# Kernel optimization log

Hardware: AMD Instinct MI355X
Metric: run time of the kernel (lower is better)

## Reference

```python
import jax, jax.numpy as jnp
import numpy as np

INPUT_DIM = 512
HIDDEN_DIM = 256
REP_DIM = 256
SCORE_HIDDEN = 128


def setup_inputs() -> dict:
    key = jax.random.key(0)
    ks = jax.random.split(key, 12)
    def rn(k, shape, scale=None):
        s = scale if scale is not None else 1.0 / np.sqrt(shape[0])
        return jax.random.normal(k, shape, dtype=jnp.float32) * s
    return {
        "feat_x": jax.random.normal(ks[0], (512, INPUT_DIM), dtype=jnp.float32),
        "feat_pos": jax.random.normal(ks[1], (512, INPUT_DIM), dtype=jnp.float32),
        "feat_neg": jax.random.normal(ks[2], (512, INPUT_DIM), dtype=jnp.float32),
        # g: Linear(input,hidden) -> GELU -> Linear(hidden,rep); stored as x @ W
        "g_w1": rn(ks[3], (INPUT_DIM, HIDDEN_DIM)),
        "g_b1": jnp.zeros((HIDDEN_DIM,), jnp.float32),
        "g_w2": rn(ks[4], (HIDDEN_DIM, REP_DIM)),
        "g_b2": jnp.zeros((REP_DIM,), jnp.float32),
        # out_proj: Linear(rep, input, bias=False)
        "out_w": rn(ks[5], (REP_DIM, INPUT_DIM)),
        # score_net: Linear(3*rep+1, score_hidden) -> GELU -> Linear(score_hidden, 1)
        "s_w1": rn(ks[6], (3 * REP_DIM + 1, SCORE_HIDDEN)),
        "s_b1": jnp.zeros((SCORE_HIDDEN,), jnp.float32),
        "s_w2": rn(ks[7], (SCORE_HIDDEN, 1)),
        "s_b2": jnp.zeros((1,), jnp.float32),
    }


def _gelu(x):
    return jax.nn.gelu(x, approximate=False)  # torch nn.GELU default = exact erf


def _g(x, g_w1, g_b1, g_w2, g_b2):
    return _gelu(x @ g_w1 + g_b1) @ g_w2 + g_b2


def _set_operator(feat_x, feat_set, params):
    g_w1, g_b1, g_w2, g_b2, out_w, s_w1, s_b1, s_w2, s_b2 = params
    x_rep = _g(feat_x, g_w1, g_b1, g_w2, g_b2)   # (n, r)
    y_rep = _g(feat_set, g_w1, g_b1, g_w2, g_b2)  # (m, r)
    n, r = x_rep.shape
    m = y_rep.shape[0]
    x_exp = jnp.broadcast_to(x_rep[:, None, :], (n, m, r))
    y_exp = jnp.broadcast_to(y_rep[None, :, :], (n, m, r))
    delta = y_exp - x_exp                                   # (n, m, r)
    delta_norm = jnp.linalg.norm(delta, axis=-1, keepdims=True)
    score_in = jnp.concatenate([x_exp, y_exp, delta, delta_norm], axis=-1)  # (n, m, 3r+1)
    logits = (_gelu(score_in @ s_w1 + s_b1) @ s_w2 + s_b2)[..., 0]          # (n, m)
    weights = jax.nn.softmax(logits, axis=1)
    set_update_rep = jnp.einsum("nm,nmr->nr", weights, delta)
    return set_update_rep @ out_w


def reference(feat_x, feat_pos, feat_neg, g_w1, g_b1, g_w2, g_b2, out_w, s_w1, s_b1, s_w2, s_b2):
    params = (g_w1, g_b1, g_w2, g_b2, out_w, s_w1, s_b1, s_w2, s_b2)
    s_pos = _set_operator(feat_x, feat_pos, params)
    s_neg = _set_operator(feat_x, feat_neg, params)  # mask_self_neg=False
    return s_pos - s_neg
```

## Files before the change

kernel.cpp:

```cpp
#include <hip/hip_runtime.h>
#include <math.h>

#define NN 512
#define IN 512
#define HD 256
#define RD 256
#define SH 128

__device__ __forceinline__ float gelu_fast(float x){
    const float z  = x * 0.70710678118654752f;
    const float az = fabsf(z);
    const float t  = __builtin_amdgcn_rcpf(fmaf(0.3275911f, az, 1.0f));
    float p = fmaf(1.061405429f, t, -1.453152027f);
    p = fmaf(p, t, 1.421413741f);
    p = fmaf(p, t, -0.284496736f);
    p = fmaf(p, t, 0.254829592f);
    p = p * t;
    const float e = __builtin_amdgcn_exp2f(z * z * -1.4426950408889634f);
    const float E = p * e;
    const float one_plus_erf = (x >= 0.0f) ? (2.0f - E) : E;
    return 0.5f * x * one_plus_erf;
}

__device__ __forceinline__ float gelu2(float u){
    const float az = fabsf(u);
    const float tt = __builtin_amdgcn_rcpf(fmaf(0.23166045f, az, 1.0f));
    float p = fmaf(1.061405429f, tt, -1.453152027f);
    p = fmaf(p, tt, 1.421413741f);
    p = fmaf(p, tt, -0.284496736f);
    p = fmaf(p, tt, 0.254829592f);
    p = p * tt;
    const float e2 = __builtin_amdgcn_exp2f(u * u * -0.72134752044448170f);
    const float Eq = p * e2;
    const float ope = (u >= 0.0f) ? (2.0f - Eq) : Eq;
    return u * ope;
}

__global__ __launch_bounds__(512) void k_rep(
    const float* __restrict__ fx, const float* __restrict__ fp, const float* __restrict__ fn,
    const float* __restrict__ w1, const float* __restrict__ b1,
    const float* __restrict__ w2, const float* __restrict__ b2,
    const float* __restrict__ s_w1,
    float* __restrict__ r_x, float* __restrict__ r_p, float* __restrict__ r_n,
    float* __restrict__ rT_p, float* __restrict__ rT_n,
    float* __restrict__ A_x, float* __restrict__ BT_p, float* __restrict__ BT_n)
{
    __shared__ float xs[4][IN];
    __shared__ float ps[8][4][HD];
    __shared__ float hs[4][HD];
    __shared__ float rloc[4][RD];
    __shared__ float ab4[4][SH];
    const int t = threadIdx.x;
    const int mat = blockIdx.x >> 7;
    const int row0 = (blockIdx.x & 127) << 2;
    const float* src = (mat==0) ? fx : (mat==1) ? fp : fn;

    {
        const int j = t >> 7, c4 = (t & 127) << 2;
        *(float4*)&xs[j][c4] = *(const float4*)&src[(row0+j)*IN + c4];
    }
    __syncthreads();

    const int cg = t & 63, s = t >> 6;
    const int c0 = cg << 2;

    {
        float4 acc[4];
        #pragma unroll
        for (int j=0;j<4;j++) acc[j] = make_float4(0.f,0.f,0.f,0.f);
        const float* wp = w1 + (s*64)*HD + c0;
        #pragma unroll 8
        for (int ii=0; ii<64; ii++){
            float4 w = *(const float4*)wp; wp += HD;
            const int i = s*64 + ii;
            #pragma unroll
            for (int j=0;j<4;j++){
                const float xv = xs[j][i];
                acc[j].x = fmaf(xv, w.x, acc[j].x);
                acc[j].y = fmaf(xv, w.y, acc[j].y);
                acc[j].z = fmaf(xv, w.z, acc[j].z);
                acc[j].w = fmaf(xv, w.w, acc[j].w);
            }
        }
        #pragma unroll
        for (int j=0;j<4;j++) *(float4*)&ps[s][j][c0] = acc[j];
    }
    __syncthreads();

    #pragma unroll
    for (int rep=0; rep<2; rep++){
        const int idx = rep*512 + t;
        const int j = idx >> 8, c = idx & 255;
        float v = b1[c];
        #pragma unroll
        for (int ss=0; ss<8; ss++) v += ps[ss][j][c];
        hs[j][c] = gelu_fast(v);
    }
    __syncthreads();

    {
        float4 acc[4];
        #pragma unroll
        for (int j=0;j<4;j++) acc[j] = make_float4(0.f,0.f,0.f,0.f);
        const float* wp = w2 + (s*32)*RD + c0;
        #pragma unroll 8
        for (int ii=0; ii<32; ii++){
            float4 w = *(const float4*)wp; wp += RD;
            const int i = s*32 + ii;
            #pragma unroll
            for (int j=0;j<4;j++){
                const float xv = hs[j][i];
                acc[j].x = fmaf(xv, w.x, acc[j].x);
                acc[j].y = fmaf(xv, w.y, acc[j].y);
                acc[j].z = fmaf(xv, w.z, acc[j].z);
                acc[j].w = fmaf(xv, w.w, acc[j].w);
            }
        }
        #pragma unroll
        for (int j=0;j<4;j++) *(float4*)&ps[s][j][c0] = acc[j];
    }
    __syncthreads();

    float* rout = (mat==0) ? r_x : (mat==1) ? r_p : r_n;
    #pragma unroll
    for (int rep=0; rep<2; rep++){
        const int idx = rep*512 + t;
        const int j = idx >> 8, c = idx & 255;
        float v = b2[c];
        #pragma unroll
        for (int ss=0; ss<8; ss++) v += ps[ss][j][c];
        rloc[j][c] = v;
        rout[(row0+j)*RD + c] = v;
    }
    __syncthreads();

    if (mat && t < 256){
        float* rT = (mat==1) ? rT_p : rT_n;
        float4 q = make_float4(rloc[0][t], rloc[1][t], rloc[2][t], rloc[3][t]);
        *(float4*)&rT[t*NN + row0] = q;
    }

    {
        const int cg2 = t & 31, s2 = t >> 5;
        const int cc0 = cg2 << 2;
        const float sgn = (mat==0) ? -1.0f : 1.0f;
        const int base1 = (mat==0) ? 0 : 256;
        const float* p1 = s_w1 + (base1 + s2*16)*SH + cc0;
        const float* p3 = s_w1 + (512   + s2*16)*SH + cc0;
        float4 a[4];
        #pragma unroll
        for (int j=0;j<4;j++) a[j] = make_float4(0.f,0.f,0.f,0.f);
        #pragma unroll 8
        for (int ii=0; ii<16; ii++){
            float4 wa = *(const float4*)p1; p1 += SH;
            float4 wd = *(const float4*)p3; p3 += SH;
            float4 w;
            w.x = fmaf(sgn, wd.x, wa.x);
            w.y = fmaf(sgn, wd.y, wa.y);
            w.z = fmaf(sgn, wd.z, wa.z);
            w.w = fmaf(sgn, wd.w, wa.w);
            const int i = s2*16 + ii;
            #pragma unroll
            for (int j=0;j<4;j++){
                const float xv = rloc[j][i];
                a[j].x = fmaf(xv, w.x, a[j].x);
                a[j].y = fmaf(xv, w.y, a[j].y);
                a[j].z = fmaf(xv, w.z, a[j].z);
                a[j].w = fmaf(xv, w.w, a[j].w);
            }
        }
        float* psf = &ps[0][0][0];
        #pragma unroll
        for (int j=0;j<4;j++) *(float4*)&psf[(s2*4 + j)*SH + cc0] = a[j];
    }
    __syncthreads();

    {
        const float* psf = &ps[0][0][0];
        const int j = t >> 7, c = t & 127;
        float v = 0.f;
        #pragma unroll
        for (int ss=0; ss<16; ss++) v += psf[(ss*4 + j)*SH + c];
        if (mat==0) A_x[(row0+j)*SH + c] = v;
        else        ab4[j][c] = v;
    }
    __syncthreads();
    if (mat && t < 128){
        float* BT = (mat==1) ? BT_p : BT_n;
        float4 q = make_float4(ab4[0][t], ab4[1][t], ab4[2][t], ab4[3][t]);
        *(float4*)&BT[t*NN + row0] = q;
    }
}

__global__ __launch_bounds__(256) void k_sd(
    const float* __restrict__ r_x, const float* __restrict__ rT_p, const float* __restrict__ rT_n,
    const float* __restrict__ A_x, const float* __restrict__ BT_p, const float* __restrict__ BT_n,
    const float* __restrict__ r_p, const float* __restrict__ r_n,
    const float* __restrict__ s_w1, const float* __restrict__ s_b1,
    const float* __restrict__ s_w2,
    float* __restrict__ psum, float* __restrict__ Spart)
{
    __shared__ float2 xs2[RD];
    __shared__ float4 cmb[SH];
    __shared__ float pda[2][128];
    __shared__ float pdb[2][128];
    __shared__ float pdc[2][128];
    __shared__ float2 evb[128];
    __shared__ float nx[2];
    __shared__ float ssum[2][2];
    const int t = threadIdx.x;
    const int set = blockIdx.x >> 10;
    const int rem = blockIdx.x & 1023;
    const int n0 = (rem >> 2) << 1;
    const int mt = rem & 3;
    const int mbase = mt << 7;
    const int tm = t & 127, kh = t >> 7;
    const int m = mbase + tm;
    const float* yT = set ? rT_n : rT_p;
    const float* BT = set ? BT_n : BT_p;

    xs2[t] = make_float2(r_x[n0*RD + t], r_x[(n0+1)*RD + t]);
    if (t < SH){
        const float b1v = s_b1[t];
        cmb[t] = make_float4(A_x[n0*SH + t] + b1v,
                             A_x[(n0+1)*SH + t] + b1v,
                             s_w1[768*SH + t],
                             0.5f * s_w2[t]);
    }
    __syncthreads();

    if (t < 128){
        const int w = t >> 6, l = t & 63;
        float v = 0.f;
        #pragma unroll
        for (int q=0;q<4;q++){
            const float2 e = xs2[l + 64*q];
            const float ev = w ? e.y : e.x;
            v = fmaf(ev, ev, v);
        }
        #pragma unroll
        for (int off=32; off>=1; off>>=1) v += __shfl_xor(v, off);
        if (l==0) nx[w] = v;
    }

    float d0=0.f, d1=0.f, ny=0.f;
    {
        const float* yp = yT + (kh << 7)*NN + m;
        #pragma unroll 16
        for (int rr=0; rr<128; rr++){
            const float y = yp[rr*NN];
            const float2 xv = xs2[(kh << 7) + rr];
            d0 = fmaf(xv.x, y, d0);
            d1 = fmaf(xv.y, y, d1);
            ny = fmaf(y, y, ny);
        }
    }
    pda[kh][tm] = d0; pdb[kh][tm] = d1; pdc[kh][tm] = ny;
    __syncthreads();
    d0 += pda[1-kh][tm]; d1 += pdb[1-kh][tm]; ny += pdc[1-kh][tm];
    const float dn0 = sqrtf(fmaxf(fmaf(-2.f, d0, nx[0] + ny), 0.f));
    const float dn1 = sqrtf(fmaxf(fmaf(-2.f, d1, nx[1] + ny), 0.f));

    float acc0 = 0.f, acc1 = 0.f;
    {
        const float* bp = BT + (kh << 6)*NN + m;
        #pragma unroll 4
        for (int kk=0; kk<64; kk++){
            const float b = bp[kk*NN];
            const float4 c = cmb[(kh << 6) + kk];
            const float u0 = fmaf(dn0, c.z, c.x + b);
            const float u1 = fmaf(dn1, c.z, c.y + b);
            acc0 = fmaf(c.w, gelu2(u0), acc0);
            acc1 = fmaf(c.w, gelu2(u1), acc1);
        }
    }
    __syncthreads();
    pda[kh][tm] = acc0; pdb[kh][tm] = acc1;
    __syncthreads();
    if (kh == 0){
        const float ev0 = __builtin_amdgcn_exp2f((acc0 + pda[1][tm]) * 1.4426950408889634f);
        const float ev1 = __builtin_amdgcn_exp2f((acc1 + pdb[1][tm]) * 1.4426950408889634f);
        evb[tm] = make_float2(ev0, ev1);
        float v0 = ev0, v1 = ev1;
        #pragma unroll
        for (int off=32; off>=1; off>>=1){ v0 += __shfl_xor(v0, off); v1 += __shfl_xor(v1, off); }
        if ((t & 63) == 0){
            ssum[tm >> 6][0] = v0;
            ssum[tm >> 6][1] = v1;
        }
    }
    __syncthreads();
    if (t < 2)
        Spart[(set*4 + mt)*NN + n0 + t] = ssum[0][t] + ssum[1][t];

    {
        const float* ry = (set ? r_n : r_p) + mbase*RD + t;
        float a0 = 0.f, a1 = 0.f;
        #pragma unroll 8
        for (int mm=0; mm<128; mm++){
            const float rv = ry[mm*RD];
            const float2 w = evb[mm];
            a0 = fmaf(w.x, rv, a0);
            a1 = fmaf(w.y, rv, a1);
        }
        float* P = psum + ((set*4 + mt)*NN + n0)*RD;
        P[t]      = a0;
        P[RD + t] = a1;
    }
}

__global__ __launch_bounds__(512) void k_fin(
    const float* __restrict__ psum, const float* __restrict__ Spart,
    const float* __restrict__ out_w, float* __restrict__ out)
{
    __shared__ float dv[2][RD];
    const int t = threadIdx.x;
    const int np = blockIdx.x >> 1, ch = blockIdx.x & 1;
    const int n0 = np << 1;

    {
        const int j = t >> 8, c = t & 255;
        const int n = n0 + j;
        float Sp = 0.f, Sn = 0.f;
        #pragma unroll
        for (int q=0;q<4;q++){
            Sp += Spart[q*NN + n];
            Sn += Spart[(4+q)*NN + n];
        }
        float vp = 0.f, vn = 0.f;
        #pragma unroll
        for (int q=0;q<4;q++){
            vp += psum[(q*NN + n)*RD + c];
            vn += psum[((4+q)*NN + n)*RD + c];
        }
        dv[j][c] = vp * (1.0f/Sp) - vn * (1.0f/Sn);
    }
    __syncthreads();

    {
        const int j = t >> 8, col = (ch << 8) + (t & 255);
        float o = 0.f;
        const float* wo = out_w + col;
        #pragma unroll 8
        for (int r=0; r<RD; r++){ o = fmaf(dv[j][r], *wo, o); wo += IN; }
        out[(n0+j)*IN + col] = o;
    }
}

extern "C" void kernel_launch(void* const* d_in, const int* in_sizes, int n_in,
                              void* d_out, int out_size, void* d_ws, size_t ws_size,
                              hipStream_t stream)
{
    const float* fx  = (const float*)d_in[0];
    const float* fp  = (const float*)d_in[1];
    const float* fn  = (const float*)d_in[2];
    const float* gw1 = (const float*)d_in[3];
    const float* gb1 = (const float*)d_in[4];
    const float* gw2 = (const float*)d_in[5];
    const float* gb2 = (const float*)d_in[6];
    const float* ow  = (const float*)d_in[7];
    const float* sw1 = (const float*)d_in[8];
    const float* sb1 = (const float*)d_in[9];
    const float* sw2 = (const float*)d_in[10];
    float* out = (float*)d_out;

    float* ws   = (float*)d_ws;
    float* r_x  = ws;
    float* r_p  = r_x  + 131072;
    float* r_n  = r_p  + 131072;
    float* rT_p = r_n  + 131072;
    float* rT_n = rT_p + 131072;
    float* A_x  = rT_n + 131072;
    float* BT_p = A_x  + 65536;
    float* BT_n = BT_p + 65536;
    float* Spar = BT_n + 65536;
    float* psum = Spar + 4096;

    hipLaunchKernelGGL(k_rep, dim3(384), dim3(512), 0, stream,
                       fx, fp, fn, gw1, gb1, gw2, gb2, sw1,
                       r_x, r_p, r_n, rT_p, rT_n, A_x, BT_p, BT_n);
    hipLaunchKernelGGL(k_sd, dim3(2048), dim3(256), 0, stream,
                       r_x, rT_p, rT_n, A_x, BT_p, BT_n, r_p, r_n,
                       sw1, sb1, sw2, psum, Spar);
    hipLaunchKernelGGL(k_fin, dim3(512), dim3(512), 0, stream,
                       psum, Spar, ow, out);
}
```

Measured before the change: 159.3 us.

## Precompute squared norms in rep kernel, halve rows per block, cheaper GELU polynomial

```diff
diff --git a/kernel.cpp b/kernel.cpp
--- a/kernel.cpp
+++ b/kernel.cpp
@@ -24,120 +24,113 @@
 
 __device__ __forceinline__ float gelu2(float u){
     const float az = fabsf(u);
-    const float tt = __builtin_amdgcn_rcpf(fmaf(0.23166045f, az, 1.0f));
-    float p = fmaf(1.061405429f, tt, -1.453152027f);
-    p = fmaf(p, tt, 1.421413741f);
-    p = fmaf(p, tt, -0.284496736f);
-    p = fmaf(p, tt, 0.254829592f);
-    p = p * tt;
+    const float tt = __builtin_amdgcn_rcpf(fmaf(0.3326725f, az, 1.0f));
+    const float P  = fmaf(fmaf(0.7478556f, tt, -0.0958798f), tt, 0.3480242f) * tt;
     const float e2 = __builtin_amdgcn_exp2f(u * u * -0.72134752044448170f);
-    const float Eq = p * e2;
+    const float Eq = P * e2;
     const float ope = (u >= 0.0f) ? (2.0f - Eq) : Eq;
     return u * ope;
 }
 
-__global__ __launch_bounds__(512) void k_rep(
+__global__ __launch_bounds__(512, 6) void k_rep(
     const float* __restrict__ fx, const float* __restrict__ fp, const float* __restrict__ fn,
     const float* __restrict__ w1, const float* __restrict__ b1,
     const float* __restrict__ w2, const float* __restrict__ b2,
     const float* __restrict__ s_w1,
     float* __restrict__ r_x, float* __restrict__ r_p, float* __restrict__ r_n,
     float* __restrict__ rT_p, float* __restrict__ rT_n,
-    float* __restrict__ A_x, float* __restrict__ BT_p, float* __restrict__ BT_n)
+    float* __restrict__ A_x, float* __restrict__ BT_p, float* __restrict__ BT_n,
+    float* __restrict__ nx2, float* __restrict__ np2, float* __restrict__ nn2)
 {
-    __shared__ float xs[4][IN];
-    __shared__ float ps[8][4][HD];
-    __shared__ float hs[4][HD];
-    __shared__ float rloc[4][RD];
-    __shared__ float ab4[4][SH];
+    __shared__ float2 xs2[IN];
+    __shared__ float ps[8][2][HD];
+    __shared__ float2 hs2[HD];
+    __shared__ float2 rl2[RD];
+    __shared__ float ab2[2][SH];
     const int t = threadIdx.x;
-    const int mat = blockIdx.x >> 7;
-    const int row0 = (blockIdx.x & 127) << 2;
+    const int mat = blockIdx.x >> 8;
+    const int row0 = (blockIdx.x & 255) << 1;
     const float* src = (mat==0) ? fx : (mat==1) ? fp : fn;
 
-    {
-        const int j = t >> 7, c4 = (t & 127) << 2;
-        *(float4*)&xs[j][c4] = *(const float4*)&src[(row0+j)*IN + c4];
-    }
+    xs2[t] = make_float2(src[row0*IN + t], src[(row0+1)*IN + t]);
     __syncthreads();
 
     const int cg = t & 63, s = t >> 6;
     const int c0 = cg << 2;
 
     {
-        float4 acc[4];
-        #pragma unroll
-        for (int j=0;j<4;j++) acc[j] = make_float4(0.f,0.f,0.f,0.f);
+        float4 a0 = make_float4(0.f,0.f,0.f,0.f), a1 = a0;
         const float* wp = w1 + (s*64)*HD + c0;
         #pragma unroll 8
         for (int ii=0; ii<64; ii++){
-            float4 w = *(const float4*)wp; wp += HD;
-            const int i = s*64 + ii;
-            #pragma unroll
-            for (int j=0;j<4;j++){
-                const float xv = xs[j][i];
-                acc[j].x = fmaf(xv, w.x, acc[j].x);
-                acc[j].y = fmaf(xv, w.y, acc[j].y);
-                acc[j].z = fmaf(xv, w.z, acc[j].z);
-                acc[j].w = fmaf(xv, w.w, acc[j].w);
-            }
-        }
-        #pragma unroll
-        for (int j=0;j<4;j++) *(float4*)&ps[s][j][c0] = acc[j];
-    }
-    __syncthreads();
-
-    #pragma unroll
-    for (int rep=0; rep<2; rep++){
-        const int idx = rep*512 + t;
-        const int j = idx >> 8, c = idx & 255;
+            const float4 w = *(const float4*)wp; wp += HD;
+            const float2 x = xs2[s*64 + ii];
+            a0.x = fmaf(x.x, w.x, a0.x); a0.y = fmaf(x.x, w.y, a0.y);
+            a0.z = fmaf(x.x, w.z, a0.z); a0.w = fmaf(x.x, w.w, a0.w);
+            a1.x = fmaf(x.y, w.x, a1.x); a1.y = fmaf(x.y, w.y, a1.y);
+            a1.z = fmaf(x.y, w.z, a1.z); a1.w = fmaf(x.y, w.w, a1.w);
+        }
+        *(float4*)&ps[s][0][c0] = a0;
+        *(float4*)&ps[s][1][c0] = a1;
+    }
+    __syncthreads();
+
+    {
+        const int j = t >> 8, c = t & 255;
         float v = b1[c];
         #pragma unroll
         for (int ss=0; ss<8; ss++) v += ps[ss][j][c];
-        hs[j][c] = gelu_fast(v);
-    }
-    __syncthreads();
-
-    {
-        float4 acc[4];
-        #pragma unroll
-        for (int j=0;j<4;j++) acc[j] = make_float4(0.f,0.f,0.f,0.f);
+        ((float*)hs2)[c*2 + j] = gelu_fast(v);
+    }
+    __syncthreads();
+
+    {
+        float4 a0 = make_float4(0.f,0.f,0.f,0.f), a1 = a0;
         const float* wp = w2 + (s*32)*RD + c0;
         #pragma unroll 8
         for (int ii=0; ii<32; ii++){
-            float4 w = *(const float4*)wp; wp += RD;
-            const int i = s*32 + ii;
-            #pragma unroll
-            for (int j=0;j<4;j++){
-                const float xv = hs[j][i];
-                acc[j].x = fmaf(xv, w.x, acc[j].x);
-                acc[j].y = fmaf(xv, w.y, acc[j].y);
-                acc[j].z = fmaf(xv, w.z, acc[j].z);
-                acc[j].w = fmaf(xv, w.w, acc[j].w);
-            }
-        }
-        #pragma unroll
-        for (int j=0;j<4;j++) *(float4*)&ps[s][j][c0] = acc[j];
-    }
-    __syncthreads();
-
-    float* rout = (mat==0) ? r_x : (mat==1) ? r_p : r_n;
-    #pragma unroll
-    for (int rep=0; rep<2; rep++){
-        const int idx = rep*512 + t;
-        const int j = idx >> 8, c = idx & 255;
+            const float4 w = *(const float4*)wp; wp += RD;
+            const float2 x = hs2[s*32 + ii];
+            a0.x = fmaf(x.x, w.x, a0.x); a0.y = fmaf(x.x, w.y, a0.y);
+            a0.z = fmaf(x.x, w.z, a0.z); a0.w = fmaf(x.x, w.w, a0.w);
+            a1.x = fmaf(x.y, w.x, a1.x); a1.y = fmaf(x.y, w.y, a1.y);
+            a1.z = fmaf(x.y, w.z, a1.z); a1.w = fmaf(x.y, w.w, a1.w);
+        }
+        *(float4*)&ps[s][0][c0] = a0;
+        *(float4*)&ps[s][1][c0] = a1;
+    }
+    __syncthreads();
+
+    {
+        const int j = t >> 8, c = t & 255;
         float v = b2[c];
         #pragma unroll
         for (int ss=0; ss<8; ss++) v += ps[ss][j][c];
-        rloc[j][c] = v;
+        ((float*)rl2)[c*2 + j] = v;
+        float* rout = (mat==0) ? r_x : (mat==1) ? r_p : r_n;
         rout[(row0+j)*RD + c] = v;
     }
     __syncthreads();
 
+    if (t < 128){
+        const int w = t >> 6, l = t & 63;
+        float v = 0.f;
+        #pragma unroll
+        for (int q=0;q<4;q++){
+            const float2 e = rl2[l + 64*q];
+            const float ev = w ? e.y : e.x;
+            v = fmaf(ev, ev, v);
+        }
+        #pragma unroll
+        for (int off=32; off>=1; off>>=1) v += __shfl_xor(v, off);
+        if (l==0){
+            float* nrm = (mat==0) ? nx2 : (mat==1) ? np2 : nn2;
+            nrm[row0 + w] = v;
+        }
+    }
     if (mat && t < 256){
         float* rT = (mat==1) ? rT_p : rT_n;
-        float4 q = make_float4(rloc[0][t], rloc[1][t], rloc[2][t], rloc[3][t]);
-        *(float4*)&rT[t*NN + row0] = q;
+        *(float2*)&rT[t*NN + row0] = rl2[t];
     }
 
     {
@@ -147,48 +140,41 @@
         const int base1 = (mat==0) ? 0 : 256;
         const float* p1 = s_w1 + (base1 + s2*16)*SH + cc0;
         const float* p3 = s_w1 + (512   + s2*16)*SH + cc0;
-        float4 a[4];
-        #pragma unroll
-        for (int j=0;j<4;j++) a[j] = make_float4(0.f,0.f,0.f,0.f);
+        float4 a0 = make_float4(0.f,0.f,0.f,0.f), a1 = a0;
         #pragma unroll 8
         for (int ii=0; ii<16; ii++){
-            float4 wa = *(const float4*)p1; p1 += SH;
-            float4 wd = *(const float4*)p3; p3 += SH;
+            const float4 wa = *(const float4*)p1; p1 += SH;
+            const float4 wd = *(const float4*)p3; p3 += SH;
             float4 w;
             w.x = fmaf(sgn, wd.x, wa.x);
             w.y = fmaf(sgn, wd.y, wa.y);
             w.z = fmaf(sgn, wd.z, wa.z);
             w.w = fmaf(sgn, wd.w, wa.w);
-            const int i = s2*16 + ii;
-            #pragma unroll
-            for (int j=0;j<4;j++){
-                const float xv = rloc[j][i];
-                a[j].x = fmaf(xv, w.x, a[j].x);
-                a[j].y = fmaf(xv, w.y, a[j].y);
-                a[j].z = fmaf(xv, w.z, a[j].z);
-                a[j].w = fmaf(xv, w.w, a[j].w);
-            }
+            const float2 x = rl2[s2*16 + ii];
+            a0.x = fmaf(x.x, w.x, a0.x); a0.y = fmaf(x.x, w.y, a0.y);
+            a0.z = fmaf(x.x, w.z, a0.z); a0.w = fmaf(x.x, w.w, a0.w);
+            a1.x = fmaf(x.y, w.x, a1.x); a1.y = fmaf(x.y, w.y, a1.y);
+            a1.z = fmaf(x.y, w.z, a1.z); a1.w = fmaf(x.y, w.w, a1.w);
         }
         float* psf = &ps[0][0][0];
-        #pragma unroll
-        for (int j=0;j<4;j++) *(float4*)&psf[(s2*4 + j)*SH + cc0] = a[j];
-    }
-    __syncthreads();
-
-    {
+        *(float4*)&psf[(s2*2+0)*SH + cc0] = a0;
+        *(float4*)&psf[(s2*2+1)*SH + cc0] = a1;
+    }
+    __syncthreads();
+
+    if (t < 256){
         const float* psf = &ps[0][0][0];
         const int j = t >> 7, c = t & 127;
         float v = 0.f;
         #pragma unroll
-        for (int ss=0; ss<16; ss++) v += psf[(ss*4 + j)*SH + c];
+        for (int ss=0; ss<16; ss++) v += psf[(ss*2+j)*SH + c];
         if (mat==0) A_x[(row0+j)*SH + c] = v;
-        else        ab4[j][c] = v;
+        else        ab2[j][c] = v;
     }
     __syncthreads();
     if (mat && t < 128){
         float* BT = (mat==1) ? BT_p : BT_n;
-        float4 q = make_float4(ab4[0][t], ab4[1][t], ab4[2][t], ab4[3][t]);
-        *(float4*)&BT[t*NN + row0] = q;
+        *(float2*)&BT[t*NN + row0] = make_float2(ab2[0][t], ab2[1][t]);
     }
 }
 
@@ -196,6 +182,7 @@
     const float* __restrict__ r_x, const float* __restrict__ rT_p, const float* __restrict__ rT_n,
     const float* __restrict__ A_x, const float* __restrict__ BT_p, const float* __restrict__ BT_n,
     const float* __restrict__ r_p, const float* __restrict__ r_n,
+    const float* __restrict__ nx2, const float* __restrict__ np2, const float* __restrict__ nn2,
     const float* __restrict__ s_w1, const float* __restrict__ s_b1,
     const float* __restrict__ s_w2,
     float* __restrict__ psum, float* __restrict__ Spart)
@@ -204,9 +191,8 @@
     __shared__ float4 cmb[SH];
     __shared__ float pda[2][128];
     __shared__ float pdb[2][128];
-    __shared__ float pdc[2][128];
+    __shared__ float ny2v[128];
     __shared__ float2 evb[128];
-    __shared__ float nx[2];
     __shared__ float ssum[2][2];
     const int t = threadIdx.x;
     const int set = blockIdx.x >> 10;
@@ -226,24 +212,13 @@
                              A_x[(n0+1)*SH + t] + b1v,
                              s_w1[768*SH + t],
                              0.5f * s_w2[t]);
-    }
-    __syncthreads();
-
-    if (t < 128){
-        const int w = t >> 6, l = t & 63;
-        float v = 0.f;
-        #pragma unroll
-        for (int q=0;q<4;q++){
-            const float2 e = xs2[l + 64*q];
-            const float ev = w ? e.y : e.x;
-            v = fmaf(ev, ev, v);
-        }
-        #pragma unroll
-        for (int off=32; off>=1; off>>=1) v += __shfl_xor(v, off);
-        if (l==0) nx[w] = v;
-    }
-
-    float d0=0.f, d1=0.f, ny=0.f;
+        ny2v[t] = (set ? nn2 : np2)[mbase + t];
+    }
+    const float nxa = nx2[n0];
+    const float nxb = nx2[n0 + 1];
+    __syncthreads();
+
+    float d0=0.f, d1=0.f;
     {
         const float* yp = yT + (kh << 7)*NN + m;
         #pragma unroll 16
@@ -252,14 +227,14 @@
             const float2 xv = xs2[(kh << 7) + rr];
             d0 = fmaf(xv.x, y, d0);
             d1 = fmaf(xv.y, y, d1);
-            ny = fmaf(y, y, ny);
-        }
-    }
-    pda[kh][tm] = d0; pdb[kh][tm] = d1; pdc[kh][tm] = ny;
-    __syncthreads();
-    d0 += pda[1-kh][tm]; d1 += pdb[1-kh][tm]; ny += pdc[1-kh][tm];
-    const float dn0 = sqrtf(fmaxf(fmaf(-2.f, d0, nx[0] + ny), 0.f));
-    const float dn1 = sqrtf(fmaxf(fmaf(-2.f, d1, nx[1] + ny), 0.f));
+        }
+    }
+    pda[kh][tm] = d0; pdb[kh][tm] = d1;
+    __syncthreads();
+    d0 += pda[1-kh][tm]; d1 += pdb[1-kh][tm];
+    const float nyc = ny2v[tm];
+    const float dn0 = sqrtf(fmaxf(fmaf(-2.f, d0, nxa + nyc), 0.f));
+    const float dn1 = sqrtf(fmaxf(fmaf(-2.f, d1, nxb + nyc), 0.f));
 
     float acc0 = 0.f, acc1 = 0.f;
     {
@@ -309,17 +284,20 @@
     }
 }
 
-__global__ __launch_bounds__(512) void k_fin(
+__global__ __launch_bounds__(256) void k_fin(
     const float* __restrict__ psum, const float* __restrict__ Spart,
     const float* __restrict__ out_w, float* __restrict__ out)
 {
     __shared__ float dv[2][RD];
     const int t = threadIdx.x;
-    const int np = blockIdx.x >> 1, ch = blockIdx.x & 1;
+    const int np = blockIdx.x >> 2, ct = blockIdx.x & 3;
     const int n0 = np << 1;
-
-    {
-        const int j = t >> 8, c = t & 255;
+    const int cb = ct << 7;
+
+    #pragma unroll
+    for (int rep=0; rep<2; rep++){
+        const int idx = rep*256 + t;
+        const int j = idx >> 8, c = idx & 255;
         const int n = n0 + j;
         float Sp = 0.f, Sn = 0.f;
         #pragma unroll
@@ -338,7 +316,8 @@
     __syncthreads();
 
     {
-        const int j = t >> 8, col = (ch << 8) + (t & 255);
+        const int j = t >> 7, cc = t & 127;
+        const int col = cb + cc;
         float o = 0.f;
         const float* wo = out_w + col;
         #pragma unroll 8
@@ -374,14 +353,18 @@
     float* BT_p = A_x  + 65536;
     float* BT_n = BT_p + 65536;
     float* Spar = BT_n + 65536;
-    float* psum = Spar + 4096;
-
-    hipLaunchKernelGGL(k_rep, dim3(384), dim3(512), 0, stream,
+    float* nx2  = Spar + 4096;
+    float* np2  = nx2  + 512;
+    float* nn2  = np2  + 512;
+    float* psum = nn2  + 512;
+
+    hipLaunchKernelGGL(k_rep, dim3(768), dim3(512), 0, stream,
                        fx, fp, fn, gw1, gb1, gw2, gb2, sw1,
-                       r_x, r_p, r_n, rT_p, rT_n, A_x, BT_p, BT_n);
+                       r_x, r_p, r_n, rT_p, rT_n, A_x, BT_p, BT_n,
+                       nx2, np2, nn2);
     hipLaunchKernelGGL(k_sd, dim3(2048), dim3(256), 0, stream,
                        r_x, rT_p, rT_n, A_x, BT_p, BT_n, r_p, r_n,
-                       sw1, sb1, sw2, psum, Spar);
-    hipLaunchKernelGGL(k_fin, dim3(512), dim3(512), 0, stream,
+                       nx2, np2, nn2, sw1, sb1, sw2, psum, Spar);
+    hipLaunchKernelGGL(k_fin, dim3(1024), dim3(256), 0, stream,
                        psum, Spar, ow, out);
 }
```

Result: slower. 166.0 us (+4.2%).
